# Optimization experiments

Measured on AMD Instinct MI355X. Metric: run time of the kernel, lower is better.

## Reference

```python
import jax, jax.numpy as jnp
import numpy as np

H, N, L, BATCH = 128, 64, 4096, 8


def _make_dplr_hippo(n):
    # HiPPO-LegS -> NPLR -> DPLR diagonalization (float64 numpy, as in torch source)
    ar = np.arange(n, dtype=np.float64)
    p0 = np.sqrt(1.0 + 2.0 * ar)
    A = p0[:, None] * p0[None, :]
    A = np.tril(A) - np.diag(ar)
    nhippo = -A
    Pv = np.sqrt(ar + 0.5)
    Bv = np.sqrt(2.0 * ar + 1.0)
    S = nhippo + Pv[:, None] * Pv[None, :]
    Lambda_real = np.mean(np.diag(S)) * np.ones(n)
    Lambda_imag, V = np.linalg.eigh(S * -1j)
    V = V.astype(np.complex64)
    P = (V.conj().T @ Pv.astype(np.complex64))
    B = (V.conj().T @ Bv.astype(np.complex64))
    Lam = (Lambda_real + 1j * Lambda_imag).astype(np.complex64)
    return Lam, P, B


def _ri(x):  # complex -> [..., 2] real view (like torch.view_as_real)
    return np.stack([x.real, x.imag], axis=-1).astype(np.float32)


def setup_inputs() -> dict:
    key = jax.random.key(0)
    k_u, k_c, k_d = jax.random.split(key, 3)
    Lam, P, B = _make_dplr_hippo(N)
    Lambda_ri = np.tile(_ri(Lam)[None], (H, 1, 1))          # [H, N, 2]
    P_ri = np.tile(_ri(P)[None], (H, 1, 1))                 # [H, N, 2]
    B_ri = np.tile(_ri(B)[None], (H, 1, 1))                 # [H, N, 2]
    C_ri = jax.random.normal(k_c, (H, N, 2), dtype=jnp.float32)
    D = jax.random.normal(k_d, (H, 1), dtype=jnp.float32)
    u = jax.random.normal(k_u, (BATCH, L, H), dtype=jnp.float32)
    step = jnp.array([1.0 / L], dtype=jnp.float32)
    return {
        "u": u,
        "B_ri": jnp.asarray(B_ri),
        "C_ri": jnp.asarray(C_ri),
        "D": D,
        "Lambda_ri": jnp.asarray(Lambda_ri),
        "P_ri": jnp.asarray(P_ri),
        "step": step,
    }


def _as_c(x_ri):
    return jax.lax.complex(x_ri[..., 0], x_ri[..., 1])


def reference(u, B_ri, C_ri, D, Lambda_ri, P_ri, step):
    Bc = _as_c(B_ri)        # [H, N] complex64
    Cc = _as_c(C_ri)        # [H, N]
    Lam = _as_c(Lambda_ri)  # [H, N]
    Pc = _as_c(P_ri)        # [H, N]
    batch, seq_len, h = u.shape

    # roots of unity and bilinear-transform terms
    z = jnp.exp(-2j * jnp.pi * jnp.arange(seq_len) / seq_len)   # [L] complex64
    g = (2.0 / step).astype(jnp.complex64) * ((1.0 - z) / (1.0 + z))  # [L]
    c = 2.0 / (1.0 + z)                                          # [L]

    # Cauchy resolvent, shared by the four cauchy_dot reductions: [H, L, N]
    r = 1.0 / (g[None, :, None] - Lam[:, None, :])

    def cauchy(v):  # v: [H, N] -> [H, L]
        return jnp.einsum("hn,hln->hl", v, r)

    k00 = cauchy(jnp.conj(Cc) * Bc)
    k01 = cauchy(jnp.conj(Cc) * Pc)
    k10 = cauchy(jnp.conj(Pc) * Bc)
    k11 = cauchy(jnp.conj(Pc) * Pc)
    at_roots = c[None, :] * (k00 - k01 * (1.0 / (1.0 + k11)) * k10)  # [H, L]

    kernel = jnp.fft.ifft(at_roots, n=seq_len, axis=-1).real  # [H, L] float32

    # linear (full) FFT convolution, length 2L-1, keep first L samples
    nfft = 2 * seq_len - 1
    u_f = jnp.fft.rfft(u, n=nfft, axis=1)                 # [B, F, H]
    k_f = jnp.fft.rfft(kernel, n=nfft, axis=-1)           # [H, F]
    y = jnp.fft.irfft(u_f * k_f.T[None], n=nfft, axis=1)[:, :seq_len, :]  # [B, L, H]

    return y + u @ D  # D: [H,1] -> broadcast add of skip term
```

## Files before the change

kernel.cpp:

```cpp
#include <hip/hip_runtime.h>
#include <hip/hip_bf16.h>
#include <hip/hip_fp16.h>
#include <math.h>

#define HH 128
#define NN 64
#define LL 4096
#define BB 8
#define NFFT 8192
#define KSTR 4160

#define CAU_BLOCKS 1024
#define TRU_BLOCKS 4096
#define SKP_BLOCKS 8192

__device__ __forceinline__ float2 cmul(float2 a, float2 b) {
    return make_float2(a.x * b.x - a.y * b.y, a.x * b.y + a.y * b.x);
}
__device__ __forceinline__ float2 cadd(float2 a, float2 b) {
    return make_float2(a.x + b.x, a.y + b.y);
}
__device__ __forceinline__ float2 csub(float2 a, float2 b) {
    return make_float2(a.x - b.x, a.y - b.y);
}
__device__ __forceinline__ int brev13(int x) { return (int)(__brev((unsigned)x) >> 19); }
__device__ __forceinline__ int kkmap(int t) {
    return (t < 4096) ? (((t & 63) << 6) | (t >> 6)) : 4096;
}
__device__ __forceinline__ int swz(int v) { return v ^ ((v >> 4) & 15); }

__device__ __forceinline__ float2 twid(float rev, float sg) {
    return make_float2(__builtin_amdgcn_cosf(rev), sg * __builtin_amdgcn_sinf(rev));
}


template <int M>
__device__ __forceinline__ void dif_f8(float2* d, int N, int tid, int nt, float sg) {
    const float inv2m = 1.0f / (2.0f * (float)M);
    const float inv4m = 1.0f / (4.0f * (float)M);
    const float inv8m = 1.0f / (8.0f * (float)M);
    const float s2 = 0.70710678118654752f;
    for (int q = tid; q < (N >> 3); q += nt) {
        int j = q & (M - 1);
        int i0 = ((q & ~(M - 1)) << 3) + j;
        float2 x0 = d[swz(i0)],         x1 = d[swz(i0 + M)],
               x2 = d[swz(i0 + 2 * M)], x3 = d[swz(i0 + 3 * M)],
               x4 = d[swz(i0 + 4 * M)], x5 = d[swz(i0 + 5 * M)],
               x6 = d[swz(i0 + 6 * M)], x7 = d[swz(i0 + 7 * M)];
        float jf = (float)j;
        float2 w8 = twid(jf * inv8m, sg);
        float2 w4 = twid(jf * inv4m, sg);
        float2 w2 = twid(jf * inv2m, sg);
        float2 e1 = make_float2(s2, sg * s2);
        float2 e3 = make_float2(-s2, sg * s2);
        float2 y0 = cadd(x0, x4), y1 = cadd(x1, x5), y2 = cadd(x2, x6), y3 = cadd(x3, x7);
        float2 t0 = csub(x0, x4), t1 = csub(x1, x5), t2 = csub(x2, x6), t3 = csub(x3, x7);
        float2 w8i = make_float2(-sg * w8.y, sg * w8.x);
        float2 z0 = cmul(w8, t0);
        float2 z1 = cmul(cmul(w8, e1), t1);
        float2 z2 = cmul(w8i, t2);
        float2 z3 = cmul(cmul(w8, e3), t3);
        {
            float2 a0 = cadd(y0, y2);
            float2 a2 = cmul(w4, csub(y0, y2));
            float2 a1 = cadd(y1, y3);
            float2 t = cmul(w4, csub(y1, y3));
            float2 a3 = make_float2(-sg * t.y, sg * t.x);
            d[swz(i0)]         = cadd(a0, a1);
            d[swz(i0 + M)]     = cmul(w2, csub(a0, a1));
            d[swz(i0 + 2 * M)] = cadd(a2, a3);
            d[swz(i0 + 3 * M)] = cmul(w2, csub(a2, a3));
        }
        {
            float2 a0 = cadd(z0, z2);
            float2 a2 = cmul(w4, csub(z0, z2));
            float2 a1 = cadd(z1, z3);
            float2 t = cmul(w4, csub(z1, z3));
            float2 a3 = make_float2(-sg * t.y, sg * t.x);
            d[swz(i0 + 4 * M)] = cadd(a0, a1);
            d[swz(i0 + 5 * M)] = cmul(w2, csub(a0, a1));
            d[swz(i0 + 6 * M)] = cadd(a2, a3);
            d[swz(i0 + 7 * M)] = cmul(w2, csub(a2, a3));
        }
    }
    __syncthreads();
}

template <int M>
__device__ __forceinline__ void dit_f8(float2* d, int N, int tid, int nt, float sg) {
    const float inv2m = 1.0f / (2.0f * (float)M);
    const float inv4m = 1.0f / (4.0f * (float)M);
    const float inv8m = 1.0f / (8.0f * (float)M);
    const float s2 = 0.70710678118654752f;
    for (int q = tid; q < (N >> 3); q += nt) {
        int j = q & (M - 1);
        int i0 = ((q & ~(M - 1)) << 3) + j;
        float2 x0 = d[swz(i0)],         x1 = d[swz(i0 + M)],
               x2 = d[swz(i0 + 2 * M)], x3 = d[swz(i0 + 3 * M)],
               x4 = d[swz(i0 + 4 * M)], x5 = d[swz(i0 + 5 * M)],
               x6 = d[swz(i0 + 6 * M)], x7 = d[swz(i0 + 7 * M)];
        float jf = (float)j;
        float2 wA = twid(jf * inv2m, sg);
        float2 wB = twid(jf * inv4m, sg);
        float2 wC = twid(jf * inv8m, sg);
        float2 t;
        t = cmul(wA, x1); float2 b0 = cadd(x0, t), b1 = csub(x0, t);
        t = cmul(wA, x3); float2 b2 = cadd(x2, t), b3 = csub(x2, t);
        t = cmul(wA, x5); float2 b4 = cadd(x4, t), b5 = csub(x4, t);
        t = cmul(wA, x7); float2 b6 = cadd(x6, t), b7 = csub(x6, t);
        float2 wBi = make_float2(-sg * wB.y, sg * wB.x);
        t = cmul(wB, b2);  float2 c0 = cadd(b0, t), c2 = csub(b0, t);
        t = cmul(wBi, b3); float2 c1 = cadd(b1, t), c3 = csub(b1, t);
        t = cmul(wB, b6);  float2 c4 = cadd(b4, t), c6 = csub(b4, t);
        t = cmul(wBi, b7); float2 c5 = cadd(b5, t), c7 = csub(b5, t);
        float2 e1 = make_float2(s2, sg * s2);
        float2 e3 = make_float2(-s2, sg * s2);
        float2 w1 = cmul(wC, e1);
        float2 w2_ = make_float2(-sg * wC.y, sg * wC.x);
        float2 w3 = cmul(wC, e3);
        t = cmul(wC, c4);  d[swz(i0)]         = cadd(c0, t); d[swz(i0 + 4 * M)] = csub(c0, t);
        t = cmul(w1, c5);  d[swz(i0 + M)]     = cadd(c1, t); d[swz(i0 + 5 * M)] = csub(c1, t);
        t = cmul(w2_, c6); d[swz(i0 + 2 * M)] = cadd(c2, t); d[swz(i0 + 6 * M)] = csub(c2, t);
        t = cmul(w3, c7);  d[swz(i0 + 3 * M)] = cadd(c3, t); d[swz(i0 + 7 * M)] = csub(c3, t);
    }
    __syncthreads();
}

__global__ __launch_bounds__(256, 8) void stage1_kernel(
    const float* __restrict__ u,
    const float* __restrict__ B_ri, const float* __restrict__ C_ri,
    const float* __restrict__ D,
    const float* __restrict__ Lambda_ri, const float* __restrict__ P_ri,
    const float* __restrict__ step,
    float2* __restrict__ at_g, float2* __restrict__ ut2, float* __restrict__ skip) {
    __shared__ float4 smem4[264];
    const int bid = blockIdx.x;
    const int tid = threadIdx.x;

    if (bid < CAU_BLOCKS) {
        float* v11f = (float*)(smem4 + 128);
        const int h = bid >> 3;
        if (tid < NN) {
            int n = tid;
            float2 C = ((const float2*)C_ri)[h * NN + n];
            float2 Bv = ((const float2*)B_ri)[h * NN + n];
            float2 P = ((const float2*)P_ri)[h * NN + n];
            float2 lam = ((const float2*)Lambda_ri)[h * NN + n];
            float2 Cc = make_float2(C.x, -C.y);
            float2 Pc = make_float2(P.x, -P.y);
            float2 v00 = cmul(Cc, Bv);
            float2 v01 = cmul(Cc, P);
            float2 v10 = cmul(Pc, Bv);
            smem4[2 * n + 0] = make_float4(lam.x, lam.y, v00.x, v00.y);
            smem4[2 * n + 1] = make_float4(v01.x, v01.y, v10.x, v10.y);
            v11f[n] = P.x * P.x + P.y * P.y;
        }
        __syncthreads();

        const int lbase = ((bid & 7) << 8) | tid;
        const float two_over_step = 2.0f / step[0];
        float gr[2], gi[2], ccx[2], ccy[2];
#pragma unroll
        for (int p = 0; p < 2; ++p) {
            int l = lbase + p * 2048;
            double th = -6.283185307179586476925286766559 * (double)l / (double)LL;
            float sn, cs;
            sincosf((float)th, &sn, &cs);
            float dr = 1.0f + cs, di = sn;
            float inv = __builtin_amdgcn_rcpf(dr * dr + di * di);
            float nr = 1.0f - cs, ni = -sn;
            gr[p] = two_over_step * (nr * dr + ni * di) * inv;
            gi[p] = two_over_step * (ni * dr - nr * di) * inv;
            ccx[p] = 2.0f * dr * inv;
            ccy[p] = -2.0f * di * inv;
        }

        float2 k00[2], k01[2], k10[2], k11[2];
#pragma unroll
        for (int p = 0; p < 2; ++p) {
            k00[p] = make_float2(0.f, 0.f);
            k01[p] = make_float2(0.f, 0.f);
            k10[p] = make_float2(0.f, 0.f);
            k11[p] = make_float2(0.f, 0.f);
        }
#pragma unroll 4
        for (int n = 0; n < NN; ++n) {
            float4 tA = smem4[2 * n + 0];
            float4 tB = smem4[2 * n + 1];
            float w11 = v11f[n];
#pragma unroll
            for (int p = 0; p < 2; ++p) {
                float ar = gr[p] - tA.x, ai = gi[p] - tA.y;
                float id = __builtin_amdgcn_rcpf(ar * ar + ai * ai);
                float2 r = make_float2(ar * id, -ai * id);
                k00[p] = cadd(k00[p], cmul(make_float2(tA.z, tA.w), r));
                k01[p] = cadd(k01[p], cmul(make_float2(tB.x, tB.y), r));
                k10[p] = cadd(k10[p], cmul(make_float2(tB.z, tB.w), r));
                k11[p].x += w11 * r.x;
                k11[p].y += w11 * r.y;
            }
        }
#pragma unroll
        for (int p = 0; p < 2; ++p) {
            float wr = 1.0f + k11[p].x, wi = k11[p].y;
            float iw = __builtin_amdgcn_rcpf(wr * wr + wi * wi);
            float2 winv = make_float2(wr * iw, -wi * iw);
            float2 t = cmul(cmul(k01[p], winv), k10[p]);
            float2 at = cmul(make_float2(ccx[p], ccy[p]),
                             make_float2(k00[p].x - t.x, k00[p].y - t.y));
            at_g[(size_t)h * LL + lbase + p * 2048] = at;
        }
    } else if (bid < CAU_BLOCKS + TRU_BLOCKS) {
        float* tile = (float*)smem4;
        int tb = bid - CAU_BLOCKS;
        int b = tb >> 9;
        int hq = (tb >> 7) & 3;
        int h0 = hq * 32;
        int l0 = (tb & 127) * 32;
        int tx = tid & 31, ty = tid >> 5;
        const float* up = u + (size_t)b * LL * HH;
        for (int i = ty; i < 32; i += 8)
            tile[i * 33 + tx] = up[(size_t)(l0 + i) * HH + h0 + tx];
        __syncthreads();
        float2* utp = ut2 + (size_t)b * 64 * LL;
#pragma unroll
        for (int i = ty; i < 16; i += 8) {
            int c = (h0 >> 1) + i;
            float2 v = make_float2(tile[tx * 33 + 2 * i], tile[tx * 33 + 2 * i + 1]);
            utp[(size_t)c * LL + l0 + tx] = v;
        }
    } else {
        int sb = bid - (CAU_BLOCKS + TRU_BLOCKS);
        int wid = tid >> 6, lane = tid & 63;
        int row = sb * 4 + wid;
        const float* ur = u + (size_t)row * HH;
        float v = ur[lane] * D[lane] + ur[lane + 64] * D[lane + 64];
        for (int off = 32; off > 0; off >>= 1) v += __shfl_down(v, off, 64);
        if (lane == 0) skip[row] = v;
    }
}

__global__ __launch_bounds__(1024) void kfreq_kernel(const float2* __restrict__ at_g,
                                                     float2* __restrict__ K01v) {
    __shared__ float2 sm[NFFT];
    const int h = blockIdx.x;
    const int tid = threadIdx.x;
    const float2* ap = at_g + (size_t)h * LL;
#pragma unroll
    for (int it = 0; it < 4; ++it) {
        int t = tid + it * 1024;
        int l = ((t & 63) << 6) | (t >> 6);
        sm[swz((int)(__brev((unsigned)l) >> 20))] = ap[l];
    }
    __syncthreads();

    dit_f8<1>(sm, 4096, tid, 1024, +1.f);
    dit_f8<8>(sm, 4096, tid, 1024, +1.f);
    dit_f8<64>(sm, 4096, tid, 1024, +1.f);
    dit_f8<512>(sm, 4096, tid, 1024, +1.f);

    const float inv8192 = 1.0f / 8192.0f;
    for (int t = tid; t < 4096; t += 1024) {
        float kv = sm[swz(t)].x * (1.0f / 4096.0f);
        float2 w = twid((float)t * inv8192, -1.f);
        sm[swz(t)] = make_float2(kv, 0.f);
        sm[swz(t + 4096)] = make_float2(kv * w.x, kv * w.y);
    }
    __syncthreads();

    dif_f8<512>(sm, 8192, tid, 1024, -1.f);
    dif_f8<64>(sm, 8192, tid, 1024, -1.f);
    dif_f8<8>(sm, 8192, tid, 1024, -1.f);
    dif_f8<1>(sm, 8192, tid, 1024, -1.f);

    float2* kp = K01v + (size_t)(h >> 1) * (2 * KSTR) + (h & 1);
    for (int t = tid; t <= 4096; t += 1024)
        kp[2 * t] = sm[swz(brev13(kkmap(t)))];
}

__global__ __launch_bounds__(1024) void conv_fft_kernel(const float2* __restrict__ ut2,
                                                        const float4* __restrict__ K01,
                                                        __half2* __restrict__ yt2) {
    __shared__ float2 sm[NFFT];
    const int b = blockIdx.x >> 6;
    const int c = blockIdx.x & 63;
    const int tid = threadIdx.x;
    const float2* up2 = ut2 + ((size_t)b * 64 + c) * LL;
    const float inv8192 = 1.0f / 8192.0f;

    for (int i = tid; i < 4096; i += 1024) {
        float2 a = up2[i];
        float2 w = twid((float)i * inv8192, -1.f);
        sm[swz(i)] = a;
        sm[swz(i + 4096)] = cmul(w, a);
    }
    __syncthreads();

    dif_f8<512>(sm, 8192, tid, 1024, -1.f);
    dif_f8<64>(sm, 8192, tid, 1024, -1.f);
    dif_f8<8>(sm, 8192, tid, 1024, -1.f);
    dif_f8<1>(sm, 8192, tid, 1024, -1.f);

    const float4* kc = K01 + (size_t)c * KSTR;
    for (int t = tid; t <= 4096; t += 1024) {
        int kk = kkmap(t);
        bool self = (kk == 0) || (kk == 4096);
        int p = swz(brev13(kk));
        int q = self ? p : swz(brev13(NFFT - kk));
        float4 kv = kc[t];
        float2 K0 = make_float2(kv.x, kv.y);
        float2 K1 = make_float2(kv.z, kv.w);
        float2 Zp = sm[p];
        float2 Zq = sm[q];
        float2 U0 = make_float2(0.5f * (Zp.x + Zq.x), 0.5f * (Zp.y - Zq.y));
        float2 U1 = make_float2(0.5f * (Zp.y + Zq.y), 0.5f * (Zq.x - Zp.x));
        float2 A = cmul(U0, K0);
        float2 C = cmul(U1, K1);
        sm[p] = make_float2(A.x - C.y, A.y + C.x);
        if (!self) sm[q] = make_float2(A.x + C.y, C.x - A.y);
    }
    __syncthreads();

    dit_f8<1>(sm, 8192, tid, 1024, +1.f);
    dit_f8<8>(sm, 8192, tid, 1024, +1.f);
    dit_f8<64>(sm, 8192, tid, 1024, +1.f);
    dit_f8<512>(sm, 8192, tid, 1024, +1.f);

    __half2* yp = yt2 + ((size_t)b * 64 + c) * LL;
    const float invN = 1.0f / (float)NFFT;
    for (int x = tid; x < 4096; x += 1024) {
        float2 w = twid((float)x * inv8192, +1.f);
        float2 a = sm[swz(x)];
        float2 bb = cmul(w, sm[swz(x + 4096)]);
        yp[x] = __floats2half2_rn((a.x + bb.x) * invN, (a.y + bb.y) * invN);
    }
}

__global__ __launch_bounds__(256) void transpose_y_kernel(const __half2* __restrict__ yt2,
                                                          const float* __restrict__ skip,
                                                          float* __restrict__ y) {
    __shared__ __half2 tile[32 * 17];
    int b = blockIdx.z;
    int c0 = blockIdx.x * 16;
    int l0 = blockIdx.y * 32;
    int tx = threadIdx.x, ty = threadIdx.y;
    const __half2* ytp = yt2 + (size_t)b * 64 * LL;
    const float* skp = skip + (size_t)b * LL;
    float* yp = y + (size_t)b * LL * HH;
    for (int i = ty; i < 16; i += 8)
        tile[tx * 17 + i] = ytp[(size_t)(c0 + i) * LL + l0 + tx];
    __syncthreads();
    int h0 = c0 * 2;
    for (int i = ty; i < 32; i += 8) {
        int l = l0 + i;
        float sk = skp[l];
        float2 f = __half22float2(tile[i * 17 + (tx >> 1)]);
        float v = (tx & 1) ? f.y : f.x;
        yp[(size_t)l * HH + h0 + tx] = v + sk;
    }
}

extern "C" void kernel_launch(void* const* d_in, const int* in_sizes, int n_in,
                              void* d_out, int out_size, void* d_ws, size_t ws_size,
                              hipStream_t stream) {
    const float* u = (const float*)d_in[0];
    const float* B_ri = (const float*)d_in[1];
    const float* C_ri = (const float*)d_in[2];
    const float* D = (const float*)d_in[3];
    const float* Lambda_ri = (const float*)d_in[4];
    const float* P_ri = (const float*)d_in[5];
    const float* step = (const float*)d_in[6];
    float* out = (float*)d_out;

    char* ws = (char*)d_ws;
    float4* K01 = (float4*)ws;
    float* skip = (float*)(ws + (size_t)6 * 1024 * 1024);
    float2* ut2 = (float2*)(ws + (size_t)8 * 1024 * 1024);
    char* hi = ws + (size_t)24 * 1024 * 1024;
    float2* at_g = (float2*)hi;
    __half2* yt2 = (__half2*)hi;

    stage1_kernel<<<dim3(CAU_BLOCKS + TRU_BLOCKS + SKP_BLOCKS), dim3(256), 0, stream>>>(
        u, B_ri, C_ri, D, Lambda_ri, P_ri, step, at_g, ut2, skip);
    kfreq_kernel<<<dim3(HH), dim3(1024), 0, stream>>>(at_g, (float2*)K01);
    conv_fft_kernel<<<dim3(BB * HH / 2), dim3(1024), 0, stream>>>(ut2, K01, yt2);
    transpose_y_kernel<<<dim3(HH / 32, LL / 32, BB), dim3(32, 8), 0, stream>>>(yt2, skip, out);
}
```

Measured before the change: 80.23 us.

## Fuse output transpose and skip add into conv FFT kernel epilogue

Drops the separate transpose kernel and the fp16 intermediate buffer. The conv FFT kernel now writes final float outputs plus the skip term straight into the [B,L,H] layout as strided float2 stores. The block index is remapped so blocks running at the same time cover neighbouring channel pairs, which should help the strided writes merge in cache. This removes one launch and an intermediate round trip through memory, at the cost of uncoalesced 8-byte stores with a stride of HH floats.

```diff
diff --git a/kernel.cpp b/kernel.cpp
--- a/kernel.cpp
+++ b/kernel.cpp
@@ -1,6 +1,5 @@
 #include <hip/hip_runtime.h>
 #include <hip/hip_bf16.h>
-#include <hip/hip_fp16.h>
 #include <math.h>
 
 #define HH 128
@@ -280,10 +279,12 @@
 
 __global__ __launch_bounds__(1024) void conv_fft_kernel(const float2* __restrict__ ut2,
                                                         const float4* __restrict__ K01,
-                                                        __half2* __restrict__ yt2) {
+                                                        const float* __restrict__ skip,
+                                                        float* __restrict__ y) {
     __shared__ float2 sm[NFFT];
-    const int b = blockIdx.x >> 6;
-    const int c = blockIdx.x & 63;
+    const int bid = blockIdx.x;
+    const int b = (bid >> 3) & 7;
+    const int c = (bid >> 6) + ((bid & 7) << 3);
     const int tid = threadIdx.x;
     const float2* up2 = ut2 + ((size_t)b * 64 + c) * LL;
     const float inv8192 = 1.0f / 8192.0f;
@@ -326,37 +327,16 @@
     dit_f8<64>(sm, 8192, tid, 1024, +1.f);
     dit_f8<512>(sm, 8192, tid, 1024, +1.f);
 
-    __half2* yp = yt2 + ((size_t)b * 64 + c) * LL;
+    float* yb = y + (size_t)b * LL * HH + 2 * c;
+    const float* skb = skip + (size_t)b * LL;
     const float invN = 1.0f / (float)NFFT;
     for (int x = tid; x < 4096; x += 1024) {
         float2 w = twid((float)x * inv8192, +1.f);
         float2 a = sm[swz(x)];
         float2 bb = cmul(w, sm[swz(x + 4096)]);
-        yp[x] = __floats2half2_rn((a.x + bb.x) * invN, (a.y + bb.y) * invN);
-    }
-}
-
-__global__ __launch_bounds__(256) void transpose_y_kernel(const __half2* __restrict__ yt2,
-                                                          const float* __restrict__ skip,
-                                                          float* __restrict__ y) {
-    __shared__ __half2 tile[32 * 17];
-    int b = blockIdx.z;
-    int c0 = blockIdx.x * 16;
-    int l0 = blockIdx.y * 32;
-    int tx = threadIdx.x, ty = threadIdx.y;
-    const __half2* ytp = yt2 + (size_t)b * 64 * LL;
-    const float* skp = skip + (size_t)b * LL;
-    float* yp = y + (size_t)b * LL * HH;
-    for (int i = ty; i < 16; i += 8)
-        tile[tx * 17 + i] = ytp[(size_t)(c0 + i) * LL + l0 + tx];
-    __syncthreads();
-    int h0 = c0 * 2;
-    for (int i = ty; i < 32; i += 8) {
-        int l = l0 + i;
-        float sk = skp[l];
-        float2 f = __half22float2(tile[i * 17 + (tx >> 1)]);
-        float v = (tx & 1) ? f.y : f.x;
-        yp[(size_t)l * HH + h0 + tx] = v + sk;
+        float sk = skb[x];
+        *(float2*)&yb[(size_t)x * HH] =
+            make_float2((a.x + bb.x) * invN + sk, (a.y + bb.y) * invN + sk);
     }
 }
 
@@ -376,13 +356,10 @@
     float4* K01 = (float4*)ws;
     float* skip = (float*)(ws + (size_t)6 * 1024 * 1024);
     float2* ut2 = (float2*)(ws + (size_t)8 * 1024 * 1024);
-    char* hi = ws + (size_t)24 * 1024 * 1024;
-    float2* at_g = (float2*)hi;
-    __half2* yt2 = (__half2*)hi;
+    float2* at_g = (float2*)(ws + (size_t)24 * 1024 * 1024);
 
     stage1_kernel<<<dim3(CAU_BLOCKS + TRU_BLOCKS + SKP_BLOCKS), dim3(256), 0, stream>>>(
         u, B_ri, C_ri, D, Lambda_ri, P_ri, step, at_g, ut2, skip);
     kfreq_kernel<<<dim3(HH), dim3(1024), 0, stream>>>(at_g, (float2*)K01);
-    conv_fft_kernel<<<dim3(BB * HH / 2), dim3(1024), 0, stream>>>(ut2, K01, yt2);
-    transpose_y_kernel<<<dim3(HH / 32, LL / 32, BB), dim3(32, 8), 0, stream>>>(yt2, skip, out);
-}
+    conv_fft_kernel<<<dim3(BB * HH / 2), dim3(1024), 0, stream>>>(ut2, K01, skip, out);
+}
```

After: 82.27 us. +2.5%, slower.
